# Kernel optimization log

Hardware: AMD Instinct MI355X
Metric: run time of the kernel (lower is better)

Reference implementation:

```python
import jax, jax.numpy as jnp
import numpy as np

NBINS = 512
TMIN, TMAX = -1.0, 1.0


def _equalize_image(image, mask):
    """Faithful jax version of HistogramEqualizer._torch_equalize_image.
    image: [C, H, W] float32; mask: [H, W] bool (the last-channel valid mask).
    Histogram is computed over masked pixels (all channels), then pixels are
    mapped through the normalized CDF via piecewise-linear interpolation.
    """
    xf = image.reshape(-1)                                   # [C*H*W]
    mf = jnp.broadcast_to(mask[None], image.shape).reshape(-1)
    # min/max over masked values only (matches torch.histc on image[:, mask])
    xmin = jnp.min(jnp.where(mf, xf, jnp.inf))
    xmax = jnp.max(jnp.where(mf, xf, -jnp.inf))
    # masked histogram: torch.histc with nbins equal-width bins over [xmin, xmax]
    t = (xf - xmin) / (xmax - xmin)
    idx = jnp.clip(jnp.floor(t * NBINS).astype(jnp.int32), 0, NBINS - 1)
    counts = jnp.zeros((NBINS,), jnp.float32).at[idx].add(mf.astype(jnp.float32))
    # bin centers: edges[:-1] + diff(edges)/2 with edges = linspace(xmin, xmax, nbins+1)
    step = (xmax - xmin) / NBINS
    centers = xmin + step * (jnp.arange(NBINS, dtype=jnp.float32) + 0.5)
    cdf = jnp.cumsum(counts)
    cdf = cdf / cdf[-1]
    # piecewise linear interp of (centers, cdf) at every pixel.
    # torch does sum(x >= centers) - 1 (O(n*nbins)); searchsorted(side='right')-1
    # is the identical index computed efficiently.
    m = (cdf[1:] - cdf[:-1]) / (centers[1:] - centers[:-1])   # [nbins-1]
    b = cdf[:-1] - m * centers[:-1]
    i = jnp.clip(jnp.searchsorted(centers, xf, side='right') - 1, 0, NBINS - 2)
    return (m[i] * xf + b[i]).reshape(image.shape)


def setup_inputs() -> dict:
    key = jax.random.key(0)
    batch = jax.random.normal(key, (16, 3, 1024, 1024), dtype=jnp.float32)
    valid_mask = jnp.ones((16, 1024, 1024), dtype=bool)
    return {"batch": batch, "valid_mask": valid_mask}


def reference(batch, valid_mask):
    # combine_valid_masks: [B,H,W] mask broadcast over channels & finiteness
    vm = valid_mask[:, None, :, :] & jnp.isfinite(batch)      # [B,C,H,W]
    # per-image equalization (per_channel=False); torch passes mask[-1] (last channel)
    eq = jax.vmap(_equalize_image)(batch, vm[:, -1])          # [B,C,H,W]
    batch_eq = jnp.where(vm, eq, jnp.nan) * (TMAX - TMIN) + TMIN
    invalid = jnp.nanmean(batch_eq, axis=(-2, -1))[:, :, None, None]  # [B,C,1,1]
    invalid = jnp.where(jnp.isfinite(invalid), invalid, jnp.nanmean(invalid))
    return jnp.where(vm, batch_eq, invalid)
```

## Files before the change

### kernel.cpp

```cpp
#include <hip/hip_runtime.h>
#include <math.h>
#include <stdint.h>


#define NBINS 512
#define HW_ (1024 * 1024)
#define G_ (HW_ / 4)
#define C_ 3
#define B_ 16
#define GPB 128
#define GROUPS_PER_BLOCK (G_ / GPB)
#define ITERS (GROUPS_PER_BLOCK / 256)
#define UNR 4

__device__ __forceinline__ unsigned enc_f(float f) {
    unsigned u = __float_as_uint(f);
    return (u & 0x80000000u) ? ~u : (u | 0x80000000u);
}
__device__ __forceinline__ float dec_f(unsigned e) {
    return __uint_as_float((e & 0x80000000u) ? (e ^ 0x80000000u) : ~e);
}


__global__ void kinit(unsigned* __restrict__ mm, unsigned* __restrict__ ghist) {
    int i = blockIdx.x * blockDim.x + threadIdx.x;
    if (i < 2 * B_) mm[i] = (i & 1) ? 0u : 0xFFFFFFFFu;
    if (i < B_ * NBINS) ghist[i] = 0u;
}

__global__ void __launch_bounds__(256) kmm(const float* __restrict__ x,
                                           const int* __restrict__ vmask,
                                           unsigned* __restrict__ mm,
                                           unsigned char* __restrict__ vbits) {
    const int b = blockIdx.y;
    const float4* __restrict__ p0 = (const float4*)(x + (size_t)b * C_ * HW_);
    const float4* __restrict__ p1 = p0 + G_;
    const float4* __restrict__ p2 = p1 + G_;
    const int4* __restrict__ mk = (const int4*)(vmask + (size_t)b * HW_);
    unsigned char* __restrict__ vb = vbits + (size_t)b * G_;
    const int base = blockIdx.x * GROUPS_PER_BLOCK + threadIdx.x;
    float lmin = INFINITY, lmax = -INFINITY;
#pragma unroll
    for (int k0 = 0; k0 < ITERS; k0 += UNR) {
        int pv[UNR];
        int4 m4[UNR];
        float4 a[UNR], c[UNR], d[UNR];
#pragma unroll
        for (int u = 0; u < UNR; u++) {
            pv[u] = base + (k0 + u) * 256;
            m4[u] = mk[pv[u]];
            a[u] = p0[pv[u]];
            c[u] = p1[pv[u]];
            d[u] = p2[pv[u]];
        }
#pragma unroll
        for (int u = 0; u < UNR; u++) {
            unsigned nib = 0;
#define PROC(MJ, AJ, CJ, DJ, BIT)                                             \
    {                                                                         \
        bool valid = ((MJ) != 0);                                             \
        if (valid) nib |= (1u << (BIT));                                      \
        bool mfl = valid && isfinite(DJ);                                     \
        lmin = fminf(lmin, mfl ? fminf(AJ, fminf(CJ, DJ)) : INFINITY);        \
        lmax = fmaxf(lmax, mfl ? fmaxf(AJ, fmaxf(CJ, DJ)) : -INFINITY);       \
    }
            PROC(m4[u].x, a[u].x, c[u].x, d[u].x, 0)
            PROC(m4[u].y, a[u].y, c[u].y, d[u].y, 1)
            PROC(m4[u].z, a[u].z, c[u].z, d[u].z, 2)
            PROC(m4[u].w, a[u].w, c[u].w, d[u].w, 3)
#undef PROC
            vb[pv[u]] = (unsigned char)nib;
        }
    }
#pragma unroll
    for (int o = 32; o > 0; o >>= 1) {
        lmin = fminf(lmin, __shfl_down(lmin, o));
        lmax = fmaxf(lmax, __shfl_down(lmax, o));
    }
    __shared__ float smin[4], smax[4];
    const int lane = threadIdx.x & 63, wid = threadIdx.x >> 6;
    if (lane == 0) {
        smin[wid] = lmin;
        smax[wid] = lmax;
    }
    __syncthreads();
    if (threadIdx.x == 0) {
        float bmin = fminf(fminf(smin[0], smin[1]), fminf(smin[2], smin[3]));
        float bmax = fmaxf(fmaxf(smax[0], smax[1]), fmaxf(smax[2], smax[3]));
        if (bmin != INFINITY) atomicMin(&mm[2 * b], enc_f(bmin));
        if (bmax != -INFINITY) atomicMax(&mm[2 * b + 1], enc_f(bmax));
    }
}

__global__ void __launch_bounds__(256) khist(const float* __restrict__ x,
                                             const unsigned char* __restrict__ vbits,
                                             const unsigned* __restrict__ mm,
                                             unsigned* __restrict__ ghist) {
    const int b = blockIdx.y;
    __shared__ unsigned lh[NBINS];
    for (int i = threadIdx.x; i < NBINS; i += 256) lh[i] = 0u;
    __syncthreads();
    const float xmin = dec_f(mm[2 * b]);
    const float xmax = dec_f(mm[2 * b + 1]);
    const float rr = 1.0f / (xmax - xmin);
    const float4* __restrict__ p0 = (const float4*)(x + (size_t)b * C_ * HW_);
    const float4* __restrict__ p1 = p0 + G_;
    const float4* __restrict__ p2 = p1 + G_;
    const unsigned char* __restrict__ vb = vbits + (size_t)b * G_;
    const int base = blockIdx.x * GROUPS_PER_BLOCK + threadIdx.x;
#pragma unroll
    for (int k0 = 0; k0 < ITERS; k0 += UNR) {
        int pv[UNR];
        unsigned nib[UNR];
        float4 a[UNR], c[UNR], d[UNR];
#pragma unroll
        for (int u = 0; u < UNR; u++) {
            pv[u] = base + (k0 + u) * 256;
            nib[u] = vb[pv[u]];
            a[u] = p0[pv[u]];
            c[u] = p1[pv[u]];
            d[u] = p2[pv[u]];
        }
#pragma unroll
        for (int u = 0; u < UNR; u++) {
#define HPROC(AJ, CJ, DJ, BIT)                                                \
    {                                                                         \
        bool mfl = ((nib[u] >> (BIT)) & 1u) && isfinite(DJ);                  \
        if (mfl) {                                                            \
            float t0 = (AJ - xmin) * rr;                                      \
            int k0i = (int)floorf(t0 * (float)NBINS);                         \
            atomicAdd(&lh[min(max(k0i, 0), NBINS - 1)], 1u);                  \
            float t1 = (CJ - xmin) * rr;                                      \
            int k1i = (int)floorf(t1 * (float)NBINS);                         \
            atomicAdd(&lh[min(max(k1i, 0), NBINS - 1)], 1u);                  \
            float t2 = (DJ - xmin) * rr;                                      \
            int k2i = (int)floorf(t2 * (float)NBINS);                         \
            atomicAdd(&lh[min(max(k2i, 0), NBINS - 1)], 1u);                  \
        }                                                                     \
    }
            HPROC(a[u].x, c[u].x, d[u].x, 0)
            HPROC(a[u].y, c[u].y, d[u].y, 1)
            HPROC(a[u].z, c[u].z, d[u].z, 2)
            HPROC(a[u].w, c[u].w, d[u].w, 3)
#undef HPROC
        }
    }
    __syncthreads();
    for (int i = threadIdx.x; i < NBINS; i += 256)
        if (lh[i]) atomicAdd(&ghist[b * NBINS + i], lh[i]);
}

__global__ void __launch_bounds__(NBINS) kcdf(const unsigned* __restrict__ mm,
                                              const unsigned* __restrict__ ghist,
                                              float* __restrict__ params,
                                              float2* __restrict__ mbt) {
    const int b = blockIdx.x;
    const int t = threadIdx.x;
    __shared__ unsigned sc[NBINS];
    __shared__ float cs[NBINS];
    sc[t] = ghist[b * NBINS + t];
    __syncthreads();
    for (int off = 1; off < NBINS; off <<= 1) {
        unsigned v = (t >= off) ? sc[t - off] : 0u;
        __syncthreads();
        sc[t] += v;
        __syncthreads();
    }
    const float total = (float)sc[NBINS - 1];
    cs[t] = (float)sc[t] / total;
    __syncthreads();
    const float xmin = dec_f(mm[2 * b]);
    const float xmax = dec_f(mm[2 * b + 1]);
    const float step = (xmax - xmin) / (float)NBINS;
    float2 mb;
    if (t < NBINS - 1) {
        float c0 = xmin + step * ((float)t + 0.5f);
        float c1 = xmin + step * ((float)t + 1.5f);
        float m = (cs[t + 1] - cs[t]) / (c1 - c0);
        mb.x = m;
        mb.y = cs[t] - m * c0;
    } else {
        mb.x = 0.0f;
        mb.y = 0.0f;
    }
    mbt[b * NBINS + t] = mb;
    if (t == 0) {
        params[2 * b] = xmin;
        params[2 * b + 1] = step;
    }
}

__device__ __forceinline__ float mapv(float v, bool valid, float xmin, float rstep,
                                      const float2* smb) {
    int i = (int)floorf((v - xmin) * rstep - 0.5f);
    i = min(max(i, 0), NBINS - 2);
    float2 mb = smb[i];
    float val = fmaf(mb.x, v, mb.y);
    return (valid && isfinite(v)) ? fmaf(val, 2.0f, -1.0f)
                                  : __uint_as_float(0x7FC00000u);
}

__global__ void __launch_bounds__(256) kmap(const float* __restrict__ x,
                                            const unsigned char* __restrict__ vbits,
                                            const float* __restrict__ params,
                                            const float2* __restrict__ mbt,
                                            float* __restrict__ out) {
    const int b = blockIdx.y;
    __shared__ float2 smb[NBINS];
    for (int i = threadIdx.x; i < NBINS; i += 256) smb[i] = mbt[b * NBINS + i];
    __syncthreads();
    const float xmin = params[2 * b];
    const float rstep = 1.0f / params[2 * b + 1];
    const float4* __restrict__ p0 = (const float4*)(x + (size_t)b * C_ * HW_);
    const float4* __restrict__ p1 = p0 + G_;
    const float4* __restrict__ p2 = p1 + G_;
    float4* __restrict__ o0 = (float4*)(out + (size_t)b * C_ * HW_);
    float4* __restrict__ o1 = o0 + G_;
    float4* __restrict__ o2 = o1 + G_;
    const unsigned char* __restrict__ vb = vbits + (size_t)b * G_;
    const int base = blockIdx.x * GROUPS_PER_BLOCK + threadIdx.x;
#pragma unroll
    for (int k0 = 0; k0 < ITERS; k0 += UNR) {
        int pv[UNR];
        unsigned nib[UNR];
        float4 a[UNR], c[UNR], d[UNR];
#pragma unroll
        for (int u = 0; u < UNR; u++) {
            pv[u] = base + (k0 + u) * 256;
            nib[u] = vb[pv[u]];
            a[u] = p0[pv[u]];
            c[u] = p1[pv[u]];
            d[u] = p2[pv[u]];
        }
#pragma unroll
        for (int u = 0; u < UNR; u++) {
            float4 ra, rc, rd;
            ra.x = mapv(a[u].x, (nib[u] >> 0) & 1u, xmin, rstep, smb);
            ra.y = mapv(a[u].y, (nib[u] >> 1) & 1u, xmin, rstep, smb);
            ra.z = mapv(a[u].z, (nib[u] >> 2) & 1u, xmin, rstep, smb);
            ra.w = mapv(a[u].w, (nib[u] >> 3) & 1u, xmin, rstep, smb);
            rc.x = mapv(c[u].x, (nib[u] >> 0) & 1u, xmin, rstep, smb);
            rc.y = mapv(c[u].y, (nib[u] >> 1) & 1u, xmin, rstep, smb);
            rc.z = mapv(c[u].z, (nib[u] >> 2) & 1u, xmin, rstep, smb);
            rc.w = mapv(c[u].w, (nib[u] >> 3) & 1u, xmin, rstep, smb);
            rd.x = mapv(d[u].x, (nib[u] >> 0) & 1u, xmin, rstep, smb);
            rd.y = mapv(d[u].y, (nib[u] >> 1) & 1u, xmin, rstep, smb);
            rd.z = mapv(d[u].z, (nib[u] >> 2) & 1u, xmin, rstep, smb);
            rd.w = mapv(d[u].w, (nib[u] >> 3) & 1u, xmin, rstep, smb);
            o0[pv[u]] = ra;
            o1[pv[u]] = rc;
            o2[pv[u]] = rd;
        }
    }
}

extern "C" void kernel_launch(void* const* d_in, const int* in_sizes, int n_in,
                              void* d_out, int out_size, void* d_ws, size_t ws_size,
                              hipStream_t stream) {
    const float* x = (const float*)d_in[0];
    const int* vmask = (const int*)d_in[1];
    float* out = (float*)d_out;

    unsigned* mm = (unsigned*)d_ws;
    unsigned* ghist = mm + 2 * B_;
    float* params = (float*)(ghist + B_ * NBINS);
    float2* mbt = (float2*)(params + 2 * B_);
    unsigned char* vbits = (unsigned char*)(mbt + B_ * NBINS);

    kinit<<<(2 * B_ + B_ * NBINS + 255) / 256, 256, 0, stream>>>(mm, ghist);
    dim3 g(GPB, B_);
    kmm<<<g, 256, 0, stream>>>(x, vmask, mm, vbits);
    khist<<<g, 256, 0, stream>>>(x, vbits, mm, ghist);
    kcdf<<<B_, NBINS, 0, stream>>>(mm, ghist, params, mbt);
    kmap<<<g, 256, 0, stream>>>(x, vbits, params, mbt, out);
}
```

Baseline: 454.0 us.

## Fuse CDF into map kernel, replicate shared histograms, add nontemporal loads and stores

Removes the separate CDF kernel: every map block now redoes the 512-bin prefix scan and builds its slope/intercept table in shared memory, which saves one launch and a global round trip at the cost of redundant per-block work. The histogram kernel spreads its shared-memory atomics over 8 padded copies to reduce contention and reduces them at the end. The mask loads in the min/max pass and the input loads and output stores in the map pass use nontemporal hints to limit cache pollution. The min/max words are split into separate arrays.

```diff
diff --git a/kernel.cpp b/kernel.cpp
--- a/kernel.cpp
+++ b/kernel.cpp
@@ -12,6 +12,24 @@
 #define GROUPS_PER_BLOCK (G_ / GPB)
 #define ITERS (GROUPS_PER_BLOCK / 256)
 #define UNR 4
+#define NCOPY 8
+#define HSTRIDE (NBINS + 1)
+
+typedef float vf4 __attribute__((ext_vector_type(4)));
+typedef int vi4 __attribute__((ext_vector_type(4)));
+
+__device__ __forceinline__ float4 ldnt_f4(const float4* p) {
+    vf4 v = __builtin_nontemporal_load((vf4*)p);
+    return make_float4(v.x, v.y, v.z, v.w);
+}
+__device__ __forceinline__ int4 ldnt_i4(const int4* p) {
+    vi4 v = __builtin_nontemporal_load((vi4*)p);
+    return make_int4(v.x, v.y, v.z, v.w);
+}
+__device__ __forceinline__ void stnt_f4(float4* p, float4 f) {
+    vf4 v = {f.x, f.y, f.z, f.w};
+    __builtin_nontemporal_store(v, (vf4*)p);
+}
 
 __device__ __forceinline__ unsigned enc_f(float f) {
     unsigned u = __float_as_uint(f);
@@ -22,15 +40,20 @@
 }
 
 
-__global__ void kinit(unsigned* __restrict__ mm, unsigned* __restrict__ ghist) {
+__global__ void kinit(unsigned* __restrict__ mm_min, unsigned* __restrict__ mm_max,
+                      unsigned* __restrict__ ghist) {
     int i = blockIdx.x * blockDim.x + threadIdx.x;
-    if (i < 2 * B_) mm[i] = (i & 1) ? 0u : 0xFFFFFFFFu;
+    if (i < B_) {
+        mm_min[i] = 0xFFFFFFFFu;
+        mm_max[i] = 0u;
+    }
     if (i < B_ * NBINS) ghist[i] = 0u;
 }
 
 __global__ void __launch_bounds__(256) kmm(const float* __restrict__ x,
                                            const int* __restrict__ vmask,
-                                           unsigned* __restrict__ mm,
+                                           unsigned* __restrict__ mm_min,
+                                           unsigned* __restrict__ mm_max,
                                            unsigned char* __restrict__ vbits) {
     const int b = blockIdx.y;
     const float4* __restrict__ p0 = (const float4*)(x + (size_t)b * C_ * HW_);
@@ -48,7 +71,7 @@
 #pragma unroll
         for (int u = 0; u < UNR; u++) {
             pv[u] = base + (k0 + u) * 256;
-            m4[u] = mk[pv[u]];
+            m4[u] = ldnt_i4(&mk[pv[u]]);
             a[u] = p0[pv[u]];
             c[u] = p1[pv[u]];
             d[u] = p2[pv[u]];
@@ -87,22 +110,24 @@
     if (threadIdx.x == 0) {
         float bmin = fminf(fminf(smin[0], smin[1]), fminf(smin[2], smin[3]));
         float bmax = fmaxf(fmaxf(smax[0], smax[1]), fmaxf(smax[2], smax[3]));
-        if (bmin != INFINITY) atomicMin(&mm[2 * b], enc_f(bmin));
-        if (bmax != -INFINITY) atomicMax(&mm[2 * b + 1], enc_f(bmax));
+        if (bmin != INFINITY) atomicMin(&mm_min[b], enc_f(bmin));
+        if (bmax != -INFINITY) atomicMax(&mm_max[b], enc_f(bmax));
     }
 }
 
 __global__ void __launch_bounds__(256) khist(const float* __restrict__ x,
                                              const unsigned char* __restrict__ vbits,
-                                             const unsigned* __restrict__ mm,
+                                             const unsigned* __restrict__ mm_min,
+                                             const unsigned* __restrict__ mm_max,
                                              unsigned* __restrict__ ghist) {
     const int b = blockIdx.y;
-    __shared__ unsigned lh[NBINS];
-    for (int i = threadIdx.x; i < NBINS; i += 256) lh[i] = 0u;
-    __syncthreads();
-    const float xmin = dec_f(mm[2 * b]);
-    const float xmax = dec_f(mm[2 * b + 1]);
+    __shared__ unsigned lh[NCOPY * HSTRIDE];
+    for (int i = threadIdx.x; i < NCOPY * HSTRIDE; i += 256) lh[i] = 0u;
+    __syncthreads();
+    const float xmin = dec_f(mm_min[b]);
+    const float xmax = dec_f(mm_max[b]);
     const float rr = 1.0f / (xmax - xmin);
+    const unsigned cbase = (threadIdx.x & (NCOPY - 1)) * HSTRIDE;
     const float4* __restrict__ p0 = (const float4*)(x + (size_t)b * C_ * HW_);
     const float4* __restrict__ p1 = p0 + G_;
     const float4* __restrict__ p2 = p1 + G_;
@@ -129,13 +154,13 @@
         if (mfl) {                                                            \
             float t0 = (AJ - xmin) * rr;                                      \
             int k0i = (int)floorf(t0 * (float)NBINS);                         \
-            atomicAdd(&lh[min(max(k0i, 0), NBINS - 1)], 1u);                  \
+            atomicAdd(&lh[cbase + min(max(k0i, 0), NBINS - 1)], 1u);          \
             float t1 = (CJ - xmin) * rr;                                      \
             int k1i = (int)floorf(t1 * (float)NBINS);                         \
-            atomicAdd(&lh[min(max(k1i, 0), NBINS - 1)], 1u);                  \
+            atomicAdd(&lh[cbase + min(max(k1i, 0), NBINS - 1)], 1u);          \
             float t2 = (DJ - xmin) * rr;                                      \
             int k2i = (int)floorf(t2 * (float)NBINS);                         \
-            atomicAdd(&lh[min(max(k2i, 0), NBINS - 1)], 1u);                  \
+            atomicAdd(&lh[cbase + min(max(k2i, 0), NBINS - 1)], 1u);          \
         }                                                                     \
     }
             HPROC(a[u].x, c[u].x, d[u].x, 0)
@@ -146,47 +171,11 @@
         }
     }
     __syncthreads();
-    for (int i = threadIdx.x; i < NBINS; i += 256)
-        if (lh[i]) atomicAdd(&ghist[b * NBINS + i], lh[i]);
-}
-
-__global__ void __launch_bounds__(NBINS) kcdf(const unsigned* __restrict__ mm,
-                                              const unsigned* __restrict__ ghist,
-                                              float* __restrict__ params,
-                                              float2* __restrict__ mbt) {
-    const int b = blockIdx.x;
-    const int t = threadIdx.x;
-    __shared__ unsigned sc[NBINS];
-    __shared__ float cs[NBINS];
-    sc[t] = ghist[b * NBINS + t];
-    __syncthreads();
-    for (int off = 1; off < NBINS; off <<= 1) {
-        unsigned v = (t >= off) ? sc[t - off] : 0u;
-        __syncthreads();
-        sc[t] += v;
-        __syncthreads();
-    }
-    const float total = (float)sc[NBINS - 1];
-    cs[t] = (float)sc[t] / total;
-    __syncthreads();
-    const float xmin = dec_f(mm[2 * b]);
-    const float xmax = dec_f(mm[2 * b + 1]);
-    const float step = (xmax - xmin) / (float)NBINS;
-    float2 mb;
-    if (t < NBINS - 1) {
-        float c0 = xmin + step * ((float)t + 0.5f);
-        float c1 = xmin + step * ((float)t + 1.5f);
-        float m = (cs[t + 1] - cs[t]) / (c1 - c0);
-        mb.x = m;
-        mb.y = cs[t] - m * c0;
-    } else {
-        mb.x = 0.0f;
-        mb.y = 0.0f;
-    }
-    mbt[b * NBINS + t] = mb;
-    if (t == 0) {
-        params[2 * b] = xmin;
-        params[2 * b + 1] = step;
+    for (int i = threadIdx.x; i < NBINS; i += 256) {
+        unsigned s = 0;
+#pragma unroll
+        for (int c2 = 0; c2 < NCOPY; c2++) s += lh[c2 * HSTRIDE + i];
+        if (s) atomicAdd(&ghist[b * NBINS + i], s);
     }
 }
 
@@ -202,15 +191,44 @@
 
 __global__ void __launch_bounds__(256) kmap(const float* __restrict__ x,
                                             const unsigned char* __restrict__ vbits,
-                                            const float* __restrict__ params,
-                                            const float2* __restrict__ mbt,
+                                            const unsigned* __restrict__ mm_min,
+                                            const unsigned* __restrict__ mm_max,
+                                            const unsigned* __restrict__ ghist,
                                             float* __restrict__ out) {
     const int b = blockIdx.y;
+    const int tid = threadIdx.x;
+    __shared__ float cs[NBINS];
     __shared__ float2 smb[NBINS];
-    for (int i = threadIdx.x; i < NBINS; i += 256) smb[i] = mbt[b * NBINS + i];
-    __syncthreads();
-    const float xmin = params[2 * b];
-    const float rstep = 1.0f / params[2 * b + 1];
+    cs[tid] = (float)ghist[b * NBINS + tid];
+    cs[tid + 256] = (float)ghist[b * NBINS + tid + 256];
+    __syncthreads();
+    const int i0 = tid, i1 = tid + 256;
+#pragma unroll
+    for (int off = 1; off < NBINS; off <<= 1) {
+        float v0 = (i0 >= off) ? cs[i0 - off] : 0.0f;
+        float v1 = (i1 >= off) ? cs[i1 - off] : 0.0f;
+        __syncthreads();
+        cs[i0] += v0;
+        cs[i1] += v1;
+        __syncthreads();
+    }
+    const float xmin = dec_f(mm_min[b]);
+    const float xmax = dec_f(mm_max[b]);
+    const float step = (xmax - xmin) / (float)NBINS;
+    const float total = cs[NBINS - 1];
+    for (int i = tid; i < NBINS - 1; i += 256) {
+        float c0 = xmin + step * ((float)i + 0.5f);
+        float c1 = xmin + step * ((float)i + 1.5f);
+        float y0 = cs[i] / total;
+        float y1 = cs[i + 1] / total;
+        float m = (y1 - y0) / (c1 - c0);
+        float2 mb;
+        mb.x = m;
+        mb.y = y0 - m * c0;
+        smb[i] = mb;
+    }
+    __syncthreads();
+    const float rstep = 1.0f / step;
     const float4* __restrict__ p0 = (const float4*)(x + (size_t)b * C_ * HW_);
     const float4* __restrict__ p1 = p0 + G_;
     const float4* __restrict__ p2 = p1 + G_;
@@ -228,9 +246,9 @@
         for (int u = 0; u < UNR; u++) {
             pv[u] = base + (k0 + u) * 256;
             nib[u] = vb[pv[u]];
-            a[u] = p0[pv[u]];
-            c[u] = p1[pv[u]];
-            d[u] = p2[pv[u]];
+            a[u] = ldnt_f4(&p0[pv[u]]);
+            c[u] = ldnt_f4(&p1[pv[u]]);
+            d[u] = ldnt_f4(&p2[pv[u]]);
         }
 #pragma unroll
         for (int u = 0; u < UNR; u++) {
@@ -247,9 +265,9 @@
             rd.y = mapv(d[u].y, (nib[u] >> 1) & 1u, xmin, rstep, smb);
             rd.z = mapv(d[u].z, (nib[u] >> 2) & 1u, xmin, rstep, smb);
             rd.w = mapv(d[u].w, (nib[u] >> 3) & 1u, xmin, rstep, smb);
-            o0[pv[u]] = ra;
-            o1[pv[u]] = rc;
-            o2[pv[u]] = rd;
+            stnt_f4(&o0[pv[u]], ra);
+            stnt_f4(&o1[pv[u]], rc);
+            stnt_f4(&o2[pv[u]], rd);
         }
     }
 }
@@ -261,16 +279,14 @@
     const int* vmask = (const int*)d_in[1];
     float* out = (float*)d_out;
 
-    unsigned* mm = (unsigned*)d_ws;
-    unsigned* ghist = mm + 2 * B_;
-    float* params = (float*)(ghist + B_ * NBINS);
-    float2* mbt = (float2*)(params + 2 * B_);
-    unsigned char* vbits = (unsigned char*)(mbt + B_ * NBINS);
-
-    kinit<<<(2 * B_ + B_ * NBINS + 255) / 256, 256, 0, stream>>>(mm, ghist);
+    unsigned* mm_min = (unsigned*)d_ws;
+    unsigned* mm_max = mm_min + B_;
+    unsigned* ghist = mm_max + B_;
+    unsigned char* vbits = (unsigned char*)(ghist + B_ * NBINS);
+
+    kinit<<<(B_ * NBINS + 255) / 256, 256, 0, stream>>>(mm_min, mm_max, ghist);
     dim3 g(GPB, B_);
-    kmm<<<g, 256, 0, stream>>>(x, vmask, mm, vbits);
-    khist<<<g, 256, 0, stream>>>(x, vbits, mm, ghist);
-    kcdf<<<B_, NBINS, 0, stream>>>(mm, ghist, params, mbt);
-    kmap<<<g, 256, 0, stream>>>(x, vbits, params, mbt, out);
-}
+    kmm<<<g, 256, 0, stream>>>(x, vmask, mm_min, mm_max, vbits);
+    khist<<<g, 256, 0, stream>>>(x, vbits, mm_min, mm_max, ghist);
+    kmap<<<g, 256, 0, stream>>>(x, vbits, mm_min, mm_max, ghist, out);
+}
```

Measured after the change: 430.8 us. 1.05x faster.
